# Optimization experiments

Hardware: AMD Instinct MI355X
Metric: run time of the kernel (lower is better)

## Reference

```python
import jax, jax.numpy as jnp
import numpy as np

HEADS = 16
CHUNK = 128  # chunked (mathematically exact) form of the causal cumsum linear attention
EPS = 0.001


def _linear_attention(q, k, v):
    # q, k, v: (B, H, L, d); q, k already SiLU-featurized
    B, H, L, d = q.shape
    Nc = L // CHUNK
    qc = q.reshape(B, H, Nc, CHUNK, d)
    kc = k.reshape(B, H, Nc, CHUNK, d)
    vc = v.reshape(B, H, Nc, CHUNK, d)

    # inter-chunk running state: S = cumsum of k (x) v over previous chunks, z = cumsum of k
    kv_chunk = jnp.einsum('bhncd,bhnce->bhnde', kc, vc)        # (B,H,Nc,d,d)
    S = jnp.cumsum(kv_chunk, axis=2) - kv_chunk                 # exclusive cumsum
    k_sum = kc.sum(axis=3)                                      # (B,H,Nc,d)
    z = jnp.cumsum(k_sum, axis=2) - k_sum                       # exclusive cumsum

    # intra-chunk causal part
    scores = jnp.einsum('bhnid,bhnjd->bhnij', qc, kc)           # (B,H,Nc,C,C)
    mask = jnp.tril(jnp.ones((CHUNK, CHUNK), dtype=bool))
    scores = jnp.where(mask, scores, jnp.zeros((), scores.dtype))
    num = jnp.einsum('bhnij,bhnje->bhnie', scores, vc)
    num = num + jnp.einsum('bhnid,bhnde->bhnie', qc, S)

    k_cum_local = jnp.cumsum(kc, axis=3)                        # within-chunk cumsum of k
    den = jnp.einsum('bhnid,bhnid->bhni', qc, k_cum_local)
    den = den + jnp.einsum('bhnid,bhnd->bhni', qc, z)

    out = num / jnp.maximum(den, EPS)[..., None]
    return out.reshape(B, H, L, d)


def setup_inputs() -> dict:
    key = jax.random.key(0)
    ks = jax.random.split(key, 9)
    D = 1024
    B, L = 4, 2048
    s = 0.02  # init scale
    return {
        'x':  jax.random.normal(ks[0], (B, L, D), dtype=jnp.float32),
        'Wq': jax.random.normal(ks[1], (D, D), dtype=jnp.float32) * s,
        'bq': jnp.zeros((D,), dtype=jnp.float32),
        'Wk': jax.random.normal(ks[2], (D, D), dtype=jnp.float32) * s,
        'bk': jnp.zeros((D,), dtype=jnp.float32),
        'Wv': jax.random.normal(ks[3], (D, D), dtype=jnp.float32) * s,
        'bv': jnp.zeros((D,), dtype=jnp.float32),
        'Wo': jax.random.normal(ks[4], (D, D), dtype=jnp.float32) * s,
        'bo': jnp.zeros((D,), dtype=jnp.float32),
    }


def reference(x, Wq, bq, Wk, bk, Wv, bv, Wo, bo):
    B, L, D = x.shape
    H = HEADS
    d = D // H
    # torch Linear: y = x @ W.T + b
    q = jax.nn.silu(x @ Wq.T + bq).reshape(B, L, H, d).transpose(0, 2, 1, 3)
    k = jax.nn.silu(x @ Wk.T + bk).reshape(B, L, H, d).transpose(0, 2, 1, 3)
    v = (x @ Wv.T + bv).reshape(B, L, H, d).transpose(0, 2, 1, 3)
    out = _linear_attention(q, k, v)                  # (B,H,L,d)
    out = out.transpose(0, 2, 1, 3).reshape(B, L, D)
    return out @ Wo.T + bo
```

## Files before the change

### kernel.cpp

```cpp
#include <hip/hip_runtime.h>
#include <math.h>

#define D_MODEL 1024
#define HEADS   16
#define HDIM    64
#define CHUNK   128
#define B_SZ    4
#define L_SEQ   2048
#define NCHUNK  16
#define NTOK    8192
#define EPS_DEN 1e-3f

typedef _Float16 half8 __attribute__((ext_vector_type(8)));
typedef _Float16 half4 __attribute__((ext_vector_type(4)));
typedef float    f32x4 __attribute__((ext_vector_type(4)));

__device__ __forceinline__ void gld_lds16(const void* g, void* l) {
    __builtin_amdgcn_global_load_lds(
        (const __attribute__((address_space(1))) void*)g,
        (__attribute__((address_space(3))) void*)l, 16, 0, 0);
}

__global__ __launch_bounds__(256) void prep(
    const float* __restrict__ x,  const float* __restrict__ Wq,
    const float* __restrict__ Wk, const float* __restrict__ Wv,
    const float* __restrict__ Wo, const float* __restrict__ bq,
    const float* __restrict__ bk,
    _Float16* __restrict__ x2,  _Float16* __restrict__ w2q,
    _Float16* __restrict__ w2k, _Float16* __restrict__ wv16,
    _Float16* __restrict__ wo16, float* __restrict__ bqk) {
    const int bid = blockIdx.x;
    if (bid < 5120) {
        const float* src; _Float16* dst; int t;
        if (bid < 4096)      { src = x;  dst = x2;  t = bid * 256 + threadIdx.x; }
        else if (bid < 4608) { src = Wq; dst = w2q; t = (bid - 4096) * 256 + threadIdx.x; }
        else                 { src = Wk; dst = w2k; t = (bid - 4608) * 256 + threadIdx.x; }
        int m = t >> 7, kc = (t & 127) << 3;
        const float* s = src + (size_t)m * 1024 + kc;
        f32x4 a = *(const f32x4*)s;
        f32x4 b = *(const f32x4*)(s + 4);
        float xs[8] = {a.x, a.y, a.z, a.w, b.x, b.y, b.z, b.w};
        half8 hi, lo;
        #pragma unroll
        for (int u = 0; u < 8; ++u) {
            _Float16 h = (_Float16)xs[u];
            hi[u] = h;
            lo[u] = (_Float16)(xs[u] - (float)h);
        }
        *(half8*)(dst + (size_t)m * 2048 + kc)        = hi;
        *(half8*)(dst + (size_t)m * 2048 + 1024 + kc) = lo;
    } else if (bid < 6144) {
        const float* src; _Float16* dst; int t;
        if (bid < 5632) { src = Wv; dst = wv16; t = (bid - 5120) * 256 + threadIdx.x; }
        else            { src = Wo; dst = wo16; t = (bid - 5632) * 256 + threadIdx.x; }
        int m = t >> 7, kc = (t & 127) << 3;
        const float* s = src + (size_t)m * 1024 + kc;
        f32x4 a = *(const f32x4*)s;
        f32x4 b = *(const f32x4*)(s + 4);
        float xs[8] = {a.x, a.y, a.z, a.w, b.x, b.y, b.z, b.w};
        half8 hv;
        #pragma unroll
        for (int u = 0; u < 8; ++u) hv[u] = (_Float16)xs[u];
        *(half8*)(dst + (size_t)m * 1024 + kc) = hv;
    } else {
        int i = (bid - 6144) * 256 + threadIdx.x;
        bqk[i] = (i < 1024) ? bq[i] : bk[i - 1024];
    }
}

__global__ __launch_bounds__(256, 4) void gemm_qkv(
    const _Float16* __restrict__ A,
    const _Float16* __restrict__ Bqk,
    const _Float16* __restrict__ Bv,
    const float* __restrict__ bqk, const float* __restrict__ bv,
    _Float16* __restrict__ Qlo, _Float16* __restrict__ Klo,
    _Float16* __restrict__ Q16, _Float16* __restrict__ K16,
    _Float16* __restrict__ V16, float* __restrict__ ksum) {
    __shared__ __align__(16) _Float16 sA[4096];
    __shared__ __align__(16) _Float16 sB[4096];
    __shared__ __align__(16) _Float16 sC16[32 * 136];
    __shared__ float sksum[2][128];

    const int cb   = blockIdx.y;
    const int isqk = (cb < 16);
    const int isk  = (cb >= 8 && cb < 16);
    const int tid  = threadIdx.x;
    const int lane = tid & 63;
    const int w    = tid >> 6;
    const int row0 = blockIdx.x * 128;
    const int col0 = cb * 128;
    const int wm   = (w & 1) * 64;
    const int wn   = (w >> 1) * 64;

    const _Float16* B = isqk ? Bqk : Bv;
    const int ldb     = isqk ? 2048 : 1024;
    const int bcol0   = isqk ? col0 : col0 - 2048;
    const int kits    = isqk ? 96 : 32;

    const int ch0 = w * 64 + lane;
    const int rS0 = ch0 >> 2;
    const int cS0 = (ch0 & 3) ^ ((rS0 >> 1) & 3);
    const int ch1 = ch0 + 256;
    const int rS1 = ch1 >> 2;
    const int cS1 = (ch1 & 3) ^ ((rS1 >> 1) & 3);

    f32x4 acc[4][4];
    #pragma unroll
    for (int i = 0; i < 4; ++i)
        #pragma unroll
        for (int j = 0; j < 4; ++j) { f32x4 z = {0.f, 0.f, 0.f, 0.f}; acc[i][j] = z; }

    const int ml = lane & 15;
    const int kg = lane >> 4;
    int offA[4], offB[4];
    #pragma unroll
    for (int i = 0; i < 4; ++i) {
        int r  = wm + i * 16 + ml;
        offA[i] = r * 32 + (kg ^ ((r >> 1) & 3)) * 8;
        int rn = wn + i * 16 + ml;
        offB[i] = rn * 32 + (kg ^ ((rn >> 1) & 3)) * 8;
    }

    for (int kit = 0; kit < kits; ++kit) {
        const int k0   = kit * 32;
        const int acol = (k0 < 2048) ? k0 : k0 - 2048;
        const int bcol = (k0 < 1024) ? k0 : k0 - 1024;

        gld_lds16(A + (size_t)(row0 + rS0) * 2048 + acol + cS0 * 8, &sA[w * 512]);
        gld_lds16(A + (size_t)(row0 + rS1) * 2048 + acol + cS1 * 8, &sA[2048 + w * 512]);
        gld_lds16(B + (size_t)(bcol0 + rS0) * ldb + bcol + cS0 * 8, &sB[w * 512]);
        gld_lds16(B + (size_t)(bcol0 + rS1) * ldb + bcol + cS1 * 8, &sB[2048 + w * 512]);
        __syncthreads();

        half8 af[4], bf[4];
        #pragma unroll
        for (int i = 0; i < 4; ++i) {
            af[i] = *(const half8*)&sA[offA[i]];
            bf[i] = *(const half8*)&sB[offB[i]];
        }
        #pragma unroll
        for (int i = 0; i < 4; ++i)
            #pragma unroll
            for (int j = 0; j < 4; ++j)
                acc[i][j] = __builtin_amdgcn_mfma_f32_16x16x32_f16(af[i], bf[j], acc[i][j], 0, 0, 0);
        __syncthreads();
    }

    const int colq = isqk ? ((col0 < 1024) ? col0 : col0 - 1024) : (col0 - 2048);
    _Float16* Ylo  = (col0 < 1024) ? Qlo : Klo;
    _Float16* Y16  = isqk ? ((col0 < 1024) ? Q16 : K16) : V16;

    const int rg = lane >> 4;
    #pragma unroll
    for (int j = 0; j < 4; ++j) {
        const float bvb = isqk ? bqk[col0 + wn + j * 16 + ml]
                               : bv[colq + wn + j * 16 + ml];
        const int nn = colq + wn + j * 16 + ml;
        #pragma unroll
        for (int i = 0; i < 4; ++i) {
            #pragma unroll
            for (int t = 0; t < 4; ++t) {
                float vv = acc[i][j][t] + bvb;
                if (isqk) {
                    vv = vv / (1.f + expf(-vv));
                    int mm = row0 + wm + i * 16 + rg * 4 + t;
                    _Float16 hv = (_Float16)vv;
                    Ylo[(size_t)mm * 1024 + nn] = (_Float16)(vv - (float)hv);
                }
                acc[i][j][t] = vv;
            }
        }
    }

    if (isk) {
        #pragma unroll
        for (int j = 0; j < 4; ++j) {
            float ps = 0.f;
            #pragma unroll
            for (int i = 0; i < 4; ++i)
                #pragma unroll
                for (int t = 0; t < 4; ++t) ps += acc[i][j][t];
            ps += __shfl_xor(ps, 16, 64);
            ps += __shfl_xor(ps, 32, 64);
            if (kg == 0) sksum[wm >> 6][wn + j * 16 + ml] = ps;
        }
        __syncthreads();
        if (tid < 128) {
            const int b = row0 >> 11;
            const int n = (row0 >> 7) & 15;
            const int cg = colq + tid;
            const int h = cg >> 6, f = cg & 63;
            ksum[(size_t)(((b * 16 + h) * 16 + n)) * 64 + f] =
                sksum[0][tid] + sksum[1][tid];
        }
        __syncthreads();
    }

    for (int s = 0; s < 4; ++s) {
        if ((wm == 0) == (s < 2)) {
            const int ib = (s & 1) * 2;
            #pragma unroll
            for (int ii = 0; ii < 2; ++ii)
                #pragma unroll
                for (int j = 0; j < 4; ++j)
                    #pragma unroll
                    for (int t = 0; t < 4; ++t) {
                        int lr = ii * 16 + rg * 4 + t;
                        sC16[lr * 136 + wn + j * 16 + ml] = (_Float16)acc[ib + ii][j][t];
                    }
        }
        __syncthreads();
        #pragma unroll
        for (int u = 0; u < 2; ++u) {
            int c = u * 256 + tid;
            int r = c >> 4, cc = (c & 15) * 8;
            half8 hv = *(const half8*)&sC16[r * 136 + cc];
            *(half8*)(Y16 + (size_t)(row0 + 32 * s + r) * 1024 + colq + cc) = hv;
        }
        __syncthreads();
    }
}

__global__ __launch_bounds__(256, 4) void gemm_out(
    const _Float16* __restrict__ A,
    const _Float16* __restrict__ B,
    const float* __restrict__ bias,
    float* __restrict__ Y) {
    __shared__ __align__(16) _Float16 sA[4096];
    __shared__ __align__(16) _Float16 sB[4096];

    const int tid  = threadIdx.x;
    const int lane = tid & 63;
    const int w    = tid >> 6;
    const int row0 = blockIdx.x * 128;
    const int col0 = blockIdx.y * 128;
    const int wm   = (w & 1) * 64;
    const int wn   = (w >> 1) * 64;

    const int ch0 = w * 64 + lane;
    const int rS0 = ch0 >> 2;
    const int cS0 = (ch0 & 3) ^ ((rS0 >> 1) & 3);
    const int ch1 = ch0 + 256;
    const int rS1 = ch1 >> 2;
    const int cS1 = (ch1 & 3) ^ ((rS1 >> 1) & 3);

    f32x4 acc[4][4];
    #pragma unroll
    for (int i = 0; i < 4; ++i)
        #pragma unroll
        for (int j = 0; j < 4; ++j) { f32x4 z = {0.f, 0.f, 0.f, 0.f}; acc[i][j] = z; }

    const int ml = lane & 15;
    const int kg = lane >> 4;
    int offA[4], offB[4];
    #pragma unroll
    for (int i = 0; i < 4; ++i) {
        int r  = wm + i * 16 + ml;
        offA[i] = r * 32 + (kg ^ ((r >> 1) & 3)) * 8;
        int rn = wn + i * 16 + ml;
        offB[i] = rn * 32 + (kg ^ ((rn >> 1) & 3)) * 8;
    }

    for (int kit = 0; kit < 32; ++kit) {
        const int k0 = kit * 32;
        gld_lds16(A + (size_t)(row0 + rS0) * 1024 + k0 + cS0 * 8, &sA[w * 512]);
        gld_lds16(A + (size_t)(row0 + rS1) * 1024 + k0 + cS1 * 8, &sA[2048 + w * 512]);
        gld_lds16(B + (size_t)(col0 + rS0) * 1024 + k0 + cS0 * 8, &sB[w * 512]);
        gld_lds16(B + (size_t)(col0 + rS1) * 1024 + k0 + cS1 * 8, &sB[2048 + w * 512]);
        __syncthreads();

        half8 af[4], bf[4];
        #pragma unroll
        for (int i = 0; i < 4; ++i) {
            af[i] = *(const half8*)&sA[offA[i]];
            bf[i] = *(const half8*)&sB[offB[i]];
        }
        #pragma unroll
        for (int i = 0; i < 4; ++i)
            #pragma unroll
            for (int j = 0; j < 4; ++j)
                acc[i][j] = __builtin_amdgcn_mfma_f32_16x16x32_f16(af[i], bf[j], acc[i][j], 0, 0, 0);
        __syncthreads();
    }

    const int rg = lane >> 4;
    #pragma unroll
    for (int j = 0; j < 4; ++j) {
        const int nn = col0 + wn + j * 16 + ml;
        const float bvb = bias[nn];
        #pragma unroll
        for (int i = 0; i < 4; ++i) {
            #pragma unroll
            for (int t = 0; t < 4; ++t) {
                int mm = row0 + wm + i * 16 + rg * 4 + t;
                Y[(size_t)mm * 1024 + nn] = acc[i][j][t] * 64.f + bvb;
            }
        }
    }
}

__global__ __launch_bounds__(256) void chunk_stats(
    const _Float16* __restrict__ k16g, const _Float16* __restrict__ v16g,
    float* __restrict__ kvT) {
    const int blk = blockIdx.x;
    const int n = blk & 15, bh = blk >> 4, h = bh & 15, b = bh >> 4;
    const size_t base = ((size_t)b * L_SEQ + (size_t)n * CHUNK) * D_MODEL + (size_t)h * HDIM;

    __shared__ __align__(16) _Float16 sv[64 * 136];
    __shared__ __align__(16) _Float16 sk[64 * 136];

    const int tid = threadIdx.x;
    #pragma unroll
    for (int p = 0; p < 4; ++p) {
        int idx = p * 256 + tid;
        int j = idx >> 3, c = idx & 7;
        half8 vv = *(const half8*)(v16g + base + (size_t)j * D_MODEL + c * 8);
        half8 kk = *(const half8*)(k16g + base + (size_t)j * D_MODEL + c * 8);
        #pragma unroll
        for (int u = 0; u < 8; ++u) {
            sv[(c * 8 + u) * 136 + j] = vv[u];
            sk[(c * 8 + u) * 136 + j] = kk[u];
        }
    }
    __syncthreads();

    const int lane = tid & 63;
    const int w    = tid >> 6;
    const int ml   = lane & 15;
    const int kg   = lane >> 4;

    f32x4 acc[4];
    #pragma unroll
    for (int ft = 0; ft < 4; ++ft) { f32x4 z = {0.f,0.f,0.f,0.f}; acc[ft] = z; }
    #pragma unroll
    for (int ft = 0; ft < 4; ++ft)
        #pragma unroll
        for (int kit = 0; kit < 4; ++kit) {
            half8 af = *(const half8*)&sv[(w * 16 + ml) * 136 + kit * 32 + kg * 8];
            half8 bf = *(const half8*)&sk[(ft * 16 + ml) * 136 + kit * 32 + kg * 8];
            acc[ft] = __builtin_amdgcn_mfma_f32_16x16x32_f16(af, bf, acc[ft], 0, 0, 0);
        }
    float* o = kvT + (size_t)blk * 4096;
    #pragma unroll
    for (int ft = 0; ft < 4; ++ft)
        #pragma unroll
        for (int t = 0; t < 4; ++t) {
            int e = w * 16 + kg * 4 + t;
            o[e * 64 + ft * 16 + ml] = acc[ft][t];
        }
}

__global__ __launch_bounds__(256) void scan_chunks(float* __restrict__ kvT,
                                                   float* __restrict__ ksum) {
    const int bh  = blockIdx.x >> 4;
    const int seg = blockIdx.x & 15;
    const int idx = seg * 256 + threadIdx.x;
    float* base = kvT + (size_t)bh * NCHUNK * 4096 + idx;
    float run = 0.f;
    #pragma unroll
    for (int nn = 0; nn < NCHUNK; ++nn) {
        float t = base[(size_t)nn * 4096];
        base[(size_t)nn * 4096] = run;
        run += t;
    }
    if (seg == 0 && threadIdx.x < 64) {
        float* zb = ksum + (size_t)bh * NCHUNK * 64 + threadIdx.x;
        float r2 = 0.f;
        #pragma unroll
        for (int nn = 0; nn < NCHUNK; ++nn) {
            float t = zb[nn * 64];
            zb[nn * 64] = r2;
            r2 += t;
        }
    }
}

__global__ __launch_bounds__(256) void attn_core(
    const _Float16* __restrict__ q16g, const _Float16* __restrict__ k16g,
    const _Float16* __restrict__ v16g, const _Float16* __restrict__ qlog,
    const _Float16* __restrict__ klog, const float* __restrict__ STg,
    const float* __restrict__ zg, _Float16* __restrict__ O16) {
    const int blk = blockIdx.x;
    const int n = blk & 15, bh = blk >> 4, h = bh & 15, b = bh >> 4;
    const size_t base = ((size_t)b * L_SEQ + (size_t)n * CHUNK) * D_MODEL + (size_t)h * HDIM;

    __shared__ __align__(16) _Float16 sq [128 * 72];
    __shared__ __align__(16) _Float16 sk [128 * 72];
    __shared__ __align__(16) _Float16 sv [64 * 136];
    __shared__ __align__(16) _Float16 sS [64 * 72];
    __shared__ __align__(16) _Float16 ssc[64 * 136];
    __shared__ float szz[64];

    const int tid = threadIdx.x;
    #pragma unroll
    for (int p = 0; p < 4; ++p) {
        int idx = p * 256 + tid;
        int j = idx >> 3, c = idx & 7;
        *(half8*)&sq[j * 72 + c * 8] = *(const half8*)(q16g + base + (size_t)j * D_MODEL + c * 8);
        *(half8*)&sk[j * 72 + c * 8] = *(const half8*)(k16g + base + (size_t)j * D_MODEL + c * 8);
        half8 vv = *(const half8*)(v16g + base + (size_t)j * D_MODEL + c * 8);
        #pragma unroll
        for (int u = 0; u < 8; ++u) sv[(c * 8 + u) * 136 + j] = vv[u];
    }
    #pragma unroll
    for (int p = 0; p < 2; ++p) {
        int idx = p * 256 + tid;
        int e = idx >> 3, c = idx & 7;
        f32x4 a = *(const f32x4*)(STg + (size_t)blk * 4096 + e * 64 + c * 8);
        f32x4 b4 = *(const f32x4*)(STg + (size_t)blk * 4096 + e * 64 + c * 8 + 4);
        half8 hv;
        hv[0] = (_Float16)a.x;  hv[1] = (_Float16)a.y;
        hv[2] = (_Float16)a.z;  hv[3] = (_Float16)a.w;
        hv[4] = (_Float16)b4.x; hv[5] = (_Float16)b4.y;
        hv[6] = (_Float16)b4.z; hv[7] = (_Float16)b4.w;
        *(half8*)&sS[e * 72 + c * 8] = hv;
    }
    if (tid < 64) szz[tid] = zg[(size_t)blk * 64 + tid];
    __syncthreads();

    const int lane = tid & 63;
    const int w    = tid >> 6;
    const int ml   = lane & 15;
    const int kg   = lane >> 4;

    for (int h2 = 0; h2 < 2; ++h2) {
        const int r0 = h2 * 64 + w * 16;
        const int rowmax = r0 + 15;

        half8 aflo[2];
        aflo[0] = *(const half8*)(qlog + base + (size_t)(r0 + ml) * D_MODEL + kg * 8);
        aflo[1] = *(const half8*)(qlog + base + (size_t)(r0 + ml) * D_MODEL + 32 + kg * 8);

        f32x4 acc1[8];
        #pragma unroll
        for (int nt = 0; nt < 8; ++nt) { f32x4 z = {0.f,0.f,0.f,0.f}; acc1[nt] = z; }
        #pragma unroll
        for (int nt = 0; nt < 8; ++nt) {
            if (nt * 16 <= rowmax) {
                #pragma unroll
                for (int kit = 0; kit < 2; ++kit) {
                    half8 af = *(const half8*)&sq[(r0 + ml) * 72 + kit * 32 + kg * 8];
                    half8 bf = *(const half8*)&sk[(nt * 16 + ml) * 72 + kit * 32 + kg * 8];
                    acc1[nt] = __builtin_amdgcn_mfma_f32_16x16x32_f16(af, bf, acc1[nt], 0, 0, 0);
                }
            }
        }
        #pragma unroll
        for (int nt = 0; nt < 8; ++nt) {
            if (nt * 16 <= rowmax) {
                const _Float16* kb = klog + base + (size_t)(nt * 16 + ml) * D_MODEL;
                half8 bl0 = *(const half8*)(kb + kg * 8);
                half8 bl1 = *(const half8*)(kb + 32 + kg * 8);
                half8 ah0 = *(const half8*)&sq[(r0 + ml) * 72 + kg * 8];
                half8 ah1 = *(const half8*)&sq[(r0 + ml) * 72 + 32 + kg * 8];
                half8 bh0 = *(const half8*)&sk[(nt * 16 + ml) * 72 + kg * 8];
                half8 bh1 = *(const half8*)&sk[(nt * 16 + ml) * 72 + 32 + kg * 8];
                acc1[nt] = __builtin_amdgcn_mfma_f32_16x16x32_f16(ah0, bl0, acc1[nt], 0, 0, 0);
                acc1[nt] = __builtin_amdgcn_mfma_f32_16x16x32_f16(ah1, bl1, acc1[nt], 0, 0, 0);
                acc1[nt] = __builtin_amdgcn_mfma_f32_16x16x32_f16(aflo[0], bh0, acc1[nt], 0, 0, 0);
                acc1[nt] = __builtin_amdgcn_mfma_f32_16x16x32_f16(aflo[1], bh1, acc1[nt], 0, 0, 0);
            }
        }

        float rs[4];
        #pragma unroll
        for (int t = 0; t < 4; ++t) {
            const int ig = r0 + kg * 4 + t;
            float s = 0.f;
            #pragma unroll
            for (int nt = 0; nt < 8; ++nt) {
                int jg = nt * 16 + ml;
                s += (jg <= ig) ? acc1[nt][t] : 0.f;
            }
            const int f0 = ml * 4;
            half4 ql = *(const half4*)(qlog + base + (size_t)ig * D_MODEL + f0);
            #pragma unroll
            for (int u = 0; u < 4; ++u)
                s += ((float)sq[ig * 72 + f0 + u] + (float)ql[u]) * szz[f0 + u];
            s += __shfl_xor(s, 1, 64);
            s += __shfl_xor(s, 2, 64);
            s += __shfl_xor(s, 4, 64);
            s += __shfl_xor(s, 8, 64);
            rs[t] = s;
        }

        #pragma unroll
        for (int nt = 0; nt < 8; ++nt) {
            #pragma unroll
            for (int t = 0; t < 4; ++t) {
                int lr = w * 16 + kg * 4 + t;
                int ig = h2 * 64 + lr;
                int jg = nt * 16 + ml;
                float val = (jg <= ig) ? acc1[nt][t] : 0.f;
                ssc[lr * 136 + jg] = (_Float16)val;
            }
        }
        __syncthreads();

        f32x4 acc2[4];
        #pragma unroll
        for (int et = 0; et < 4; ++et) { f32x4 z = {0.f,0.f,0.f,0.f}; acc2[et] = z; }
        const int nkit = (h2 == 0) ? 2 : 4;
        #pragma unroll
        for (int et = 0; et < 4; ++et) {
            for (int kit = 0; kit < nkit; ++kit) {
                half8 af = *(const half8*)&ssc[(w * 16 + ml) * 136 + kit * 32 + kg * 8];
                half8 bf = *(const half8*)&sv[(et * 16 + ml) * 136 + kit * 32 + kg * 8];
                acc2[et] = __builtin_amdgcn_mfma_f32_16x16x32_f16(af, bf, acc2[et], 0, 0, 0);
            }
            #pragma unroll
            for (int kit = 0; kit < 2; ++kit) {
                half8 af = *(const half8*)&sq[(r0 + ml) * 72 + kit * 32 + kg * 8];
                half8 bf = *(const half8*)&sS[(et * 16 + ml) * 72 + kit * 32 + kg * 8];
                acc2[et] = __builtin_amdgcn_mfma_f32_16x16x32_f16(af, bf, acc2[et], 0, 0, 0);
            }
        }
        #pragma unroll
        for (int t = 0; t < 4; ++t) {
            int lr = w * 16 + kg * 4 + t;
            int ig = h2 * 64 + lr;
            float rc = 0.015625f / fmaxf(rs[t], EPS_DEN);
            #pragma unroll
            for (int et = 0; et < 4; ++et) {
                int e = et * 16 + ml;
                O16[base + (size_t)ig * D_MODEL + e] = (_Float16)(acc2[et][t] * rc);
            }
        }
        __syncthreads();
    }
}

extern "C" void kernel_launch(void* const* d_in, const int* in_sizes, int n_in,
                              void* d_out, int out_size, void* d_ws, size_t ws_size,
                              hipStream_t stream) {
    const float* x  = (const float*)d_in[0];
    const float* Wq = (const float*)d_in[1];
    const float* bq = (const float*)d_in[2];
    const float* Wk = (const float*)d_in[3];
    const float* bk = (const float*)d_in[4];
    const float* Wv = (const float*)d_in[5];
    const float* bv = (const float*)d_in[6];
    const float* Wo = (const float*)d_in[7];
    const float* bo = (const float*)d_in[8];
    float* out = (float*)d_out;

    char* p = (char*)d_ws;
    _Float16* x2   = (_Float16*)p;  p += (size_t)NTOK * 2048 * 2;
    _Float16* w2q  = (_Float16*)p;  p += (size_t)1024 * 2048 * 2;
    _Float16* w2k  = (_Float16*)p;  p += (size_t)1024 * 2048 * 2;
    _Float16* wv16 = (_Float16*)p;  p += (size_t)1024 * 1024 * 2;
    _Float16* wo16 = (_Float16*)p;  p += (size_t)1024 * 1024 * 2;
    _Float16* qlo  = (_Float16*)p;  p += (size_t)NTOK * 1024 * 2;
    _Float16* klo  = (_Float16*)p;  p += (size_t)NTOK * 1024 * 2;
    _Float16* q16  = (_Float16*)p;  p += (size_t)NTOK * 1024 * 2;
    _Float16* k16  = (_Float16*)p;  p += (size_t)NTOK * 1024 * 2;
    _Float16* v16  = (_Float16*)p;  p += (size_t)NTOK * 1024 * 2;
    float* kvT  = (float*)p;        p += (size_t)1024 * 4096 * 4;
    float* ksb  = (float*)p;        p += (size_t)1024 * 64 * 4;
    float* bqk  = (float*)p;        p += 2048 * 4;
    _Float16* attn16 = x2;

    prep<<<6152, 256, 0, stream>>>(x, Wq, Wk, Wv, Wo, bq, bk,
                                   x2, w2q, w2k, wv16, wo16, bqk);

    gemm_qkv<<<dim3(64, 24), 256, 0, stream>>>(x2, w2q, wv16, bqk, bv,
                                               qlo, klo, q16, k16, v16, ksb);

    chunk_stats<<<1024, 256, 0, stream>>>(k16, v16, kvT);
    scan_chunks<<<1024, 256, 0, stream>>>(kvT, ksb);
    attn_core<<<1024, 256, 0, stream>>>(q16, k16, v16, qlo, klo, kvT, ksb, attn16);

    gemm_out<<<dim3(64, 8), 256, 0, stream>>>(attn16, wo16, bo, out);
}
```

Measured before the change: 346.6 us.

## Restructure QKV GEMM into 256x256 tiles with triple-buffered async LDS pipeline

The QKV projection kernel moves from 128x128 tiles with 256 threads to 256x256 tiles with 512 threads. Each block computes a Q or K tile and then a 128-column V tile, which reuses the A rows and shrinks the grid to 256 blocks. The K loop now uses a three-slot LDS ring filled by global_load_lds, with manual vmcnt waits, split staging between MFMA halves, and setprio around the MFMA bursts, so loads overlap compute. The aim is higher arithmetic intensity and hidden memory latency. The cost is heavier register pressure (128 accumulator floats per thread), fewer blocks than CUs, and fragile hand-written barrier and waitcnt logic.

```diff
diff --git a/kernel.cpp b/kernel.cpp
--- a/kernel.cpp
+++ b/kernel.cpp
@@ -68,7 +68,7 @@
     }
 }
 
-__global__ __launch_bounds__(256, 4) void gemm_qkv(
+__global__ __launch_bounds__(512, 2) void gemm_qkv(
     const _Float16* __restrict__ A,
     const _Float16* __restrict__ Bqk,
     const _Float16* __restrict__ Bv,
@@ -76,148 +76,262 @@
     _Float16* __restrict__ Qlo, _Float16* __restrict__ Klo,
     _Float16* __restrict__ Q16, _Float16* __restrict__ K16,
     _Float16* __restrict__ V16, float* __restrict__ ksum) {
-    __shared__ __align__(16) _Float16 sA[4096];
-    __shared__ __align__(16) _Float16 sB[4096];
-    __shared__ __align__(16) _Float16 sC16[32 * 136];
-    __shared__ float sksum[2][128];
-
-    const int cb   = blockIdx.y;
-    const int isqk = (cb < 16);
-    const int isk  = (cb >= 8 && cb < 16);
+    __shared__ __align__(16) _Float16 sbuf[3 * 16384];
+
     const int tid  = threadIdx.x;
     const int lane = tid & 63;
     const int w    = tid >> 6;
-    const int row0 = blockIdx.x * 128;
-    const int col0 = cb * 128;
-    const int wm   = (w & 1) * 64;
+    const int bx   = blockIdx.x;
+    const int cb   = blockIdx.y;
+    const int row0 = bx * 256;
+    const int col0 = cb * 256;
+    const int isk  = (cb >= 4);
+    const int wm   = (w & 1) * 128;
     const int wn   = (w >> 1) * 64;
-
-    const _Float16* B = isqk ? Bqk : Bv;
-    const int ldb     = isqk ? 2048 : 1024;
-    const int bcol0   = isqk ? col0 : col0 - 2048;
-    const int kits    = isqk ? 96 : 32;
-
-    const int ch0 = w * 64 + lane;
-    const int rS0 = ch0 >> 2;
-    const int cS0 = (ch0 & 3) ^ ((rS0 >> 1) & 3);
-    const int ch1 = ch0 + 256;
-    const int rS1 = ch1 >> 2;
-    const int cS1 = (ch1 & 3) ^ ((rS1 >> 1) & 3);
-
-    f32x4 acc[4][4];
-    #pragma unroll
-    for (int i = 0; i < 4; ++i)
-        #pragma unroll
-        for (int j = 0; j < 4; ++j) { f32x4 z = {0.f, 0.f, 0.f, 0.f}; acc[i][j] = z; }
-
-    const int ml = lane & 15;
-    const int kg = lane >> 4;
-    int offA[4], offB[4];
-    #pragma unroll
-    for (int i = 0; i < 4; ++i) {
-        int r  = wm + i * 16 + ml;
+    const int wnv  = (w >> 1) * 32;
+    const int ml   = lane & 15;
+    const int kg   = lane >> 4;
+
+    const int rS = tid >> 2;
+    const int cS = (tid & 3) ^ ((rS >> 1) & 3);
+    const _Float16* gA0 = A   + (size_t)(row0 + rS) * 2048 + cS * 8;
+    const _Float16* gA1 = gA0 + (size_t)128 * 2048;
+    const _Float16* gB0 = Bqk + (size_t)(col0 + rS) * 2048 + cS * 8;
+    const _Float16* gB1 = gB0 + (size_t)128 * 2048;
+    const _Float16* gBv = Bv  + (size_t)(cb * 128 + rS) * 1024 + cS * 8;
+
+    int offA[8], offB[4], offBv[2];
+    #pragma unroll
+    for (int i = 0; i < 8; ++i) {
+        int r = wm + i * 16 + ml;
         offA[i] = r * 32 + (kg ^ ((r >> 1) & 3)) * 8;
-        int rn = wn + i * 16 + ml;
-        offB[i] = rn * 32 + (kg ^ ((rn >> 1) & 3)) * 8;
-    }
-
-    for (int kit = 0; kit < kits; ++kit) {
-        const int k0   = kit * 32;
+    }
+    #pragma unroll
+    for (int j = 0; j < 4; ++j) {
+        int rn = wn + j * 16 + ml;
+        offB[j] = 8192 + rn * 32 + (kg ^ ((rn >> 1) & 3)) * 8;
+    }
+    #pragma unroll
+    for (int j = 0; j < 2; ++j) {
+        int rn = wnv + j * 16 + ml;
+        offBv[j] = 8192 + rn * 32 + (kg ^ ((rn >> 1) & 3)) * 8;
+    }
+
+    f32x4 acc[8][4];
+    #pragma unroll
+    for (int i = 0; i < 8; ++i)
+        #pragma unroll
+        for (int j = 0; j < 4; ++j) { f32x4 z = {0.f,0.f,0.f,0.f}; acc[i][j] = z; }
+
+    auto stageQK_A = [&](int t, int slot) {
+        const int k0 = t * 32;
         const int acol = (k0 < 2048) ? k0 : k0 - 2048;
+        _Float16* l = sbuf + slot * 16384 + w * 512;
+        gld_lds16(gA0 + acol, l);
+        gld_lds16(gA1 + acol, l + 4096);
+    };
+    auto stageQK_B = [&](int t, int slot) {
+        const int k0 = t * 32;
         const int bcol = (k0 < 1024) ? k0 : k0 - 1024;
-
-        gld_lds16(A + (size_t)(row0 + rS0) * 2048 + acol + cS0 * 8, &sA[w * 512]);
-        gld_lds16(A + (size_t)(row0 + rS1) * 2048 + acol + cS1 * 8, &sA[2048 + w * 512]);
-        gld_lds16(B + (size_t)(bcol0 + rS0) * ldb + bcol + cS0 * 8, &sB[w * 512]);
-        gld_lds16(B + (size_t)(bcol0 + rS1) * ldb + bcol + cS1 * 8, &sB[2048 + w * 512]);
-        __syncthreads();
-
+        _Float16* l = sbuf + slot * 16384 + w * 512;
+        gld_lds16(gB0 + bcol, l + 8192);
+        gld_lds16(gB1 + bcol, l + 12288);
+    };
+
+    stageQK_A(0, 0); stageQK_B(0, 0);
+    stageQK_A(1, 1); stageQK_B(1, 1);
+    int slr = 0, sln = 2;
+    for (int t = 0; t < 96; ++t) {
+        if (t + 1 < 96) asm volatile("s_waitcnt vmcnt(4)\n\ts_barrier" ::: "memory");
+        else            asm volatile("s_waitcnt vmcnt(0)\n\ts_barrier" ::: "memory");
+        const _Float16* lb = sbuf + slr * 16384;
         half8 af[4], bf[4];
         #pragma unroll
-        for (int i = 0; i < 4; ++i) {
-            af[i] = *(const half8*)&sA[offA[i]];
-            bf[i] = *(const half8*)&sB[offB[i]];
-        }
+        for (int i = 0; i < 4; ++i) af[i] = *(const half8*)&lb[offA[i]];
+        #pragma unroll
+        for (int j = 0; j < 4; ++j) bf[j] = *(const half8*)&lb[offB[j]];
+        if (t + 2 < 96) stageQK_A(t + 2, sln);
+        asm volatile("s_barrier" ::: "memory");
+        __builtin_amdgcn_s_setprio(1);
         #pragma unroll
         for (int i = 0; i < 4; ++i)
             #pragma unroll
             for (int j = 0; j < 4; ++j)
                 acc[i][j] = __builtin_amdgcn_mfma_f32_16x16x32_f16(af[i], bf[j], acc[i][j], 0, 0, 0);
-        __syncthreads();
-    }
-
-    const int colq = isqk ? ((col0 < 1024) ? col0 : col0 - 1024) : (col0 - 2048);
-    _Float16* Ylo  = (col0 < 1024) ? Qlo : Klo;
-    _Float16* Y16  = isqk ? ((col0 < 1024) ? Q16 : K16) : V16;
-
-    const int rg = lane >> 4;
+        __builtin_amdgcn_s_setprio(0);
+        asm volatile("s_barrier" ::: "memory");
+        half8 ag[4];
+        #pragma unroll
+        for (int i = 0; i < 4; ++i) ag[i] = *(const half8*)&lb[offA[4 + i]];
+        if (t + 2 < 96) stageQK_B(t + 2, sln);
+        asm volatile("s_barrier" ::: "memory");
+        __builtin_amdgcn_s_setprio(1);
+        #pragma unroll
+        for (int i = 0; i < 4; ++i)
+            #pragma unroll
+            for (int j = 0; j < 4; ++j)
+                acc[4 + i][j] = __builtin_amdgcn_mfma_f32_16x16x32_f16(ag[i], bf[j], acc[4 + i][j], 0, 0, 0);
+        __builtin_amdgcn_s_setprio(0);
+        slr = (slr == 2) ? 0 : slr + 1;
+        sln = (sln == 2) ? 0 : sln + 1;
+    }
+
+    auto stageV_A = [&](int t, int slot) {
+        const int k0 = t * 32;
+        _Float16* l = sbuf + slot * 16384 + w * 512;
+        gld_lds16(gA0 + k0, l);
+        gld_lds16(gA1 + k0, l + 4096);
+    };
+    auto stageV_B = [&](int t, int slot) {
+        gld_lds16(gBv + t * 32, sbuf + slot * 16384 + 8192 + w * 512);
+    };
+    stageV_A(0, 0); stageV_B(0, 0);
+    stageV_A(1, 1); stageV_B(1, 1);
+
+    const int colq = isk ? col0 - 1024 : col0;
+    _Float16* Ylo  = isk ? Klo : Qlo;
+    _Float16* Y16  = isk ? K16 : Q16;
+
     #pragma unroll
     for (int j = 0; j < 4; ++j) {
-        const float bvb = isqk ? bqk[col0 + wn + j * 16 + ml]
-                               : bv[colq + wn + j * 16 + ml];
+        const float bvb = bqk[col0 + wn + j * 16 + ml];
         const int nn = colq + wn + j * 16 + ml;
         #pragma unroll
-        for (int i = 0; i < 4; ++i) {
-            #pragma unroll
-            for (int t = 0; t < 4; ++t) {
-                float vv = acc[i][j][t] + bvb;
-                if (isqk) {
-                    vv = vv / (1.f + expf(-vv));
-                    int mm = row0 + wm + i * 16 + rg * 4 + t;
-                    _Float16 hv = (_Float16)vv;
-                    Ylo[(size_t)mm * 1024 + nn] = (_Float16)(vv - (float)hv);
-                }
-                acc[i][j][t] = vv;
+        for (int i = 0; i < 8; ++i) {
+            #pragma unroll
+            for (int tt = 0; tt < 4; ++tt) {
+                float vv = acc[i][j][tt] + bvb;
+                vv = vv / (1.f + expf(-vv));
+                int mm = row0 + wm + i * 16 + kg * 4 + tt;
+                _Float16 hv = (_Float16)vv;
+                Ylo[(size_t)mm * 1024 + nn] = (_Float16)(vv - (float)hv);
+                acc[i][j][tt] = vv;
             }
         }
     }
 
     if (isk) {
+        const int bb = (row0 + wm) >> 11;
+        const int nc = ((row0 + wm) >> 7) & 15;
         #pragma unroll
         for (int j = 0; j < 4; ++j) {
             float ps = 0.f;
             #pragma unroll
-            for (int i = 0; i < 4; ++i)
+            for (int i = 0; i < 8; ++i)
                 #pragma unroll
-                for (int t = 0; t < 4; ++t) ps += acc[i][j][t];
+                for (int tt = 0; tt < 4; ++tt) ps += acc[i][j][tt];
             ps += __shfl_xor(ps, 16, 64);
             ps += __shfl_xor(ps, 32, 64);
-            if (kg == 0) sksum[wm >> 6][wn + j * 16 + ml] = ps;
-        }
-        __syncthreads();
-        if (tid < 128) {
-            const int b = row0 >> 11;
-            const int n = (row0 >> 7) & 15;
-            const int cg = colq + tid;
-            const int h = cg >> 6, f = cg & 63;
-            ksum[(size_t)(((b * 16 + h) * 16 + n)) * 64 + f] =
-                sksum[0][tid] + sksum[1][tid];
-        }
-        __syncthreads();
-    }
-
-    for (int s = 0; s < 4; ++s) {
-        if ((wm == 0) == (s < 2)) {
-            const int ib = (s & 1) * 2;
-            #pragma unroll
-            for (int ii = 0; ii < 2; ++ii)
+            if (kg == 0) {
+                const int cg = colq + wn + j * 16 + ml;
+                const int h = cg >> 6, f = cg & 63;
+                ksum[(size_t)((bb * 16 + h) * 16 + nc) * 64 + f] = ps;
+            }
+        }
+    }
+
+    {
+        _Float16* sl = sbuf + 32768;
+        asm volatile("s_barrier" ::: "memory");
+        for (int s = 0; s < 8; ++s) {
+            if ((w & 1) == (s >> 2)) {
+                const int i0 = (s & 3) * 2;
                 #pragma unroll
-                for (int j = 0; j < 4; ++j)
+                for (int ii = 0; ii < 2; ++ii)
                     #pragma unroll
-                    for (int t = 0; t < 4; ++t) {
-                        int lr = ii * 16 + rg * 4 + t;
-                        sC16[lr * 136 + wn + j * 16 + ml] = (_Float16)acc[ib + ii][j][t];
-                    }
-        }
-        __syncthreads();
-        #pragma unroll
-        for (int u = 0; u < 2; ++u) {
-            int c = u * 256 + tid;
-            int r = c >> 4, cc = (c & 15) * 8;
-            half8 hv = *(const half8*)&sC16[r * 136 + cc];
-            *(half8*)(Y16 + (size_t)(row0 + 32 * s + r) * 1024 + colq + cc) = hv;
-        }
-        __syncthreads();
+                    for (int j = 0; j < 4; ++j)
+                        #pragma unroll
+                        for (int tt = 0; tt < 4; ++tt) {
+                            int lr = ii * 16 + kg * 4 + tt;
+                            sl[lr * 264 + wn + j * 16 + ml] = (_Float16)acc[i0 + ii][j][tt];
+                        }
+            }
+            __syncthreads();
+            {
+                const int r = tid >> 4, c0 = (tid & 15) * 16;
+                half8 h0 = *(const half8*)&sl[r * 264 + c0];
+                half8 h1 = *(const half8*)&sl[r * 264 + c0 + 8];
+                *(half8*)(Y16 + (size_t)(row0 + s * 32 + r) * 1024 + colq + c0)     = h0;
+                *(half8*)(Y16 + (size_t)(row0 + s * 32 + r) * 1024 + colq + c0 + 8) = h1;
+            }
+            __syncthreads();
+        }
+    }
+
+    f32x4 vacc[8][2];
+    #pragma unroll
+    for (int i = 0; i < 8; ++i)
+        #pragma unroll
+        for (int j = 0; j < 2; ++j) { f32x4 z = {0.f,0.f,0.f,0.f}; vacc[i][j] = z; }
+
+    slr = 0; sln = 2;
+    for (int t = 0; t < 32; ++t) {
+        if (t + 1 < 32) asm volatile("s_waitcnt vmcnt(3)\n\ts_barrier" ::: "memory");
+        else            asm volatile("s_waitcnt vmcnt(0)\n\ts_barrier" ::: "memory");
+        const _Float16* lb = sbuf + slr * 16384;
+        half8 af[4], bf[2];
+        #pragma unroll
+        for (int i = 0; i < 4; ++i) af[i] = *(const half8*)&lb[offA[i]];
+        #pragma unroll
+        for (int j = 0; j < 2; ++j) bf[j] = *(const half8*)&lb[offBv[j]];
+        if (t + 2 < 32) stageV_A(t + 2, sln);
+        asm volatile("s_barrier" ::: "memory");
+        __builtin_amdgcn_s_setprio(1);
+        #pragma unroll
+        for (int i = 0; i < 4; ++i)
+            #pragma unroll
+            for (int j = 0; j < 2; ++j)
+                vacc[i][j] = __builtin_amdgcn_mfma_f32_16x16x32_f16(af[i], bf[j], vacc[i][j], 0, 0, 0);
+        __builtin_amdgcn_s_setprio(0);
+        asm volatile("s_barrier" ::: "memory");
+        half8 ag[4];
+        #pragma unroll
+        for (int i = 0; i < 4; ++i) ag[i] = *(const half8*)&lb[offA[4 + i]];
+        if (t + 2 < 32) stageV_B(t + 2, sln);
+        asm volatile("s_barrier" ::: "memory");
+        __builtin_amdgcn_s_setprio(1);
+        #pragma unroll
+        for (int i = 0; i < 4; ++i)
+            #pragma unroll
+            for (int j = 0; j < 2; ++j)
+                vacc[4 + i][j] = __builtin_amdgcn_mfma_f32_16x16x32_f16(ag[i], bf[j], vacc[4 + i][j], 0, 0, 0);
+        __builtin_amdgcn_s_setprio(0);
+        slr = (slr == 2) ? 0 : slr + 1;
+        sln = (sln == 2) ? 0 : sln + 1;
+    }
+
+    #pragma unroll
+    for (int j = 0; j < 2; ++j) {
+        const float bvb = bv[cb * 128 + wnv + j * 16 + ml];
+        #pragma unroll
+        for (int i = 0; i < 8; ++i)
+            #pragma unroll
+            for (int tt = 0; tt < 4; ++tt) vacc[i][j][tt] += bvb;
+    }
+    {
+        _Float16* sl = sbuf + 32768;
+        asm volatile("s_barrier" ::: "memory");
+        for (int s = 0; s < 8; ++s) {
+            if ((w & 1) == (s >> 2)) {
+                const int i0 = (s & 3) * 2;
+                #pragma unroll
+                for (int ii = 0; ii < 2; ++ii)
+                    #pragma unroll
+                    for (int j = 0; j < 2; ++j)
+                        #pragma unroll
+                        for (int tt = 0; tt < 4; ++tt) {
+                            int lr = ii * 16 + kg * 4 + tt;
+                            sl[lr * 136 + wnv + j * 16 + ml] = (_Float16)vacc[i0 + ii][j][tt];
+                        }
+            }
+            __syncthreads();
+            {
+                const int r = tid >> 4, c0 = (tid & 15) * 8;
+                half8 h0 = *(const half8*)&sl[r * 136 + c0];
+                *(half8*)(V16 + (size_t)(row0 + s * 32 + r) * 1024 + cb * 128 + c0) = h0;
+            }
+            __syncthreads();
+        }
     }
 }
 
@@ -563,8 +677,8 @@
     prep<<<6152, 256, 0, stream>>>(x, Wq, Wk, Wv, Wo, bq, bk,
                                    x2, w2q, w2k, wv16, wo16, bqk);
 
-    gemm_qkv<<<dim3(64, 24), 256, 0, stream>>>(x2, w2q, wv16, bqk, bv,
-                                               qlo, klo, q16, k16, v16, ksb);
+    gemm_qkv<<<dim3(32, 8), 512, 0, stream>>>(x2, w2q, wv16, bqk, bv,
+                                              qlo, klo, q16, k16, v16, ksb);
 
     chunk_stats<<<1024, 256, 0, stream>>>(k16, v16, kvT);
     scan_chunks<<<1024, 256, 0, stream>>>(kvT, ksb);
```

Result: slower. 355.8 us (+2.7%).

## Double-buffer LDS tiles in QKV and output GEMMs to overlap loads with MFMA

Applied to the files above, without the earlier changes.

Both GEMM kernels now use two LDS buffers and issue the direct global-to-LDS loads for the next k-tile before running the MFMAs on the current tile. Each iteration then ends with a single vmcnt wait plus barrier instead of two __syncthreads. This is meant to hide global load latency behind matrix math. s_setprio is also raised around the MFMA block. LDS use per block doubles to 32KB, which may limit occupancy under the 4-blocks-per-CU launch bound. There is also a possible hazard from reading the current buffer while the epilogue's sC16 aliases the same LDS.

```diff
diff --git a/kernel.cpp b/kernel.cpp
--- a/kernel.cpp
+++ b/kernel.cpp
@@ -76,10 +76,9 @@
     _Float16* __restrict__ Qlo, _Float16* __restrict__ Klo,
     _Float16* __restrict__ Q16, _Float16* __restrict__ K16,
     _Float16* __restrict__ V16, float* __restrict__ ksum) {
-    __shared__ __align__(16) _Float16 sA[4096];
-    __shared__ __align__(16) _Float16 sB[4096];
-    __shared__ __align__(16) _Float16 sC16[32 * 136];
+    __shared__ __align__(16) _Float16 sbuf[2 * 8192];
     __shared__ float sksum[2][128];
+    _Float16* sC16 = sbuf;
 
     const int cb   = blockIdx.y;
     const int isqk = (cb < 16);
@@ -104,6 +103,22 @@
     const int rS1 = ch1 >> 2;
     const int cS1 = (ch1 & 3) ^ ((rS1 >> 1) & 3);
 
+    const _Float16* gA0 = A + (size_t)(row0  + rS0) * 2048 + cS0 * 8;
+    const _Float16* gA1 = A + (size_t)(row0  + rS1) * 2048 + cS1 * 8;
+    const _Float16* gB0 = B + (size_t)(bcol0 + rS0) * ldb  + cS0 * 8;
+    const _Float16* gB1 = B + (size_t)(bcol0 + rS1) * ldb  + cS1 * 8;
+
+    auto stage = [&](int kt, int bsel) {
+        const int k0   = kt * 32;
+        const int acol = (k0 < 2048) ? k0 : k0 - 2048;
+        const int bcol = (k0 < 1024) ? k0 : k0 - 1024;
+        _Float16* l = sbuf + bsel * 8192;
+        gld_lds16(gA0 + acol, l + w * 512);
+        gld_lds16(gA1 + acol, l + 2048 + w * 512);
+        gld_lds16(gB0 + bcol, l + 4096 + w * 512);
+        gld_lds16(gB1 + bcol, l + 6144 + w * 512);
+    };
+
     f32x4 acc[4][4];
     #pragma unroll
     for (int i = 0; i < 4; ++i)
@@ -118,32 +133,30 @@
         int r  = wm + i * 16 + ml;
         offA[i] = r * 32 + (kg ^ ((r >> 1) & 3)) * 8;
         int rn = wn + i * 16 + ml;
-        offB[i] = rn * 32 + (kg ^ ((rn >> 1) & 3)) * 8;
-    }
-
-    for (int kit = 0; kit < kits; ++kit) {
-        const int k0   = kit * 32;
-        const int acol = (k0 < 2048) ? k0 : k0 - 2048;
-        const int bcol = (k0 < 1024) ? k0 : k0 - 1024;
-
-        gld_lds16(A + (size_t)(row0 + rS0) * 2048 + acol + cS0 * 8, &sA[w * 512]);
-        gld_lds16(A + (size_t)(row0 + rS1) * 2048 + acol + cS1 * 8, &sA[2048 + w * 512]);
-        gld_lds16(B + (size_t)(bcol0 + rS0) * ldb + bcol + cS0 * 8, &sB[w * 512]);
-        gld_lds16(B + (size_t)(bcol0 + rS1) * ldb + bcol + cS1 * 8, &sB[2048 + w * 512]);
-        __syncthreads();
-
+        offB[i] = 4096 + rn * 32 + (kg ^ ((rn >> 1) & 3)) * 8;
+    }
+
+    stage(0, 0);
+    asm volatile("s_waitcnt vmcnt(0)\n\ts_barrier" ::: "memory");
+    int cur = 0;
+    for (int t = 0; t < kits; ++t) {
+        if (t + 1 < kits) stage(t + 1, cur ^ 1);
+        const _Float16* lb = sbuf + cur * 8192;
         half8 af[4], bf[4];
         #pragma unroll
         for (int i = 0; i < 4; ++i) {
-            af[i] = *(const half8*)&sA[offA[i]];
-            bf[i] = *(const half8*)&sB[offB[i]];
-        }
+            af[i] = *(const half8*)&lb[offA[i]];
+            bf[i] = *(const half8*)&lb[offB[i]];
+        }
+        __builtin_amdgcn_s_setprio(1);
         #pragma unroll
         for (int i = 0; i < 4; ++i)
             #pragma unroll
             for (int j = 0; j < 4; ++j)
                 acc[i][j] = __builtin_amdgcn_mfma_f32_16x16x32_f16(af[i], bf[j], acc[i][j], 0, 0, 0);
-        __syncthreads();
+        __builtin_amdgcn_s_setprio(0);
+        asm volatile("s_waitcnt vmcnt(0)\n\ts_barrier" ::: "memory");
+        cur ^= 1;
     }
 
     const int colq = isqk ? ((col0 < 1024) ? col0 : col0 - 1024) : (col0 - 2048);
@@ -226,8 +239,7 @@
     const _Float16* __restrict__ B,
     const float* __restrict__ bias,
     float* __restrict__ Y) {
-    __shared__ __align__(16) _Float16 sA[4096];
-    __shared__ __align__(16) _Float16 sB[4096];
+    __shared__ __align__(16) _Float16 sbuf[2 * 8192];
 
     const int tid  = threadIdx.x;
     const int lane = tid & 63;
@@ -244,6 +256,20 @@
     const int rS1 = ch1 >> 2;
     const int cS1 = (ch1 & 3) ^ ((rS1 >> 1) & 3);
 
+    const _Float16* gA0 = A + (size_t)(row0 + rS0) * 1024 + cS0 * 8;
+    const _Float16* gA1 = A + (size_t)(row0 + rS1) * 1024 + cS1 * 8;
+    const _Float16* gB0 = B + (size_t)(col0 + rS0) * 1024 + cS0 * 8;
+    const _Float16* gB1 = B + (size_t)(col0 + rS1) * 1024 + cS1 * 8;
+
+    auto stage = [&](int kt, int bsel) {
+        const int k0 = kt * 32;
+        _Float16* l = sbuf + bsel * 8192;
+        gld_lds16(gA0 + k0, l + w * 512);
+        gld_lds16(gA1 + k0, l + 2048 + w * 512);
+        gld_lds16(gB0 + k0, l + 4096 + w * 512);
+        gld_lds16(gB1 + k0, l + 6144 + w * 512);
+    };
+
     f32x4 acc[4][4];
     #pragma unroll
     for (int i = 0; i < 4; ++i)
@@ -258,29 +284,30 @@
         int r  = wm + i * 16 + ml;
         offA[i] = r * 32 + (kg ^ ((r >> 1) & 3)) * 8;
         int rn = wn + i * 16 + ml;
-        offB[i] = rn * 32 + (kg ^ ((rn >> 1) & 3)) * 8;
-    }
-
+        offB[i] = 4096 + rn * 32 + (kg ^ ((rn >> 1) & 3)) * 8;
+    }
+
+    stage(0, 0);
+    asm volatile("s_waitcnt vmcnt(0)\n\ts_barrier" ::: "memory");
+    int cur = 0;
     for (int kit = 0; kit < 32; ++kit) {
-        const int k0 = kit * 32;
-        gld_lds16(A + (size_t)(row0 + rS0) * 1024 + k0 + cS0 * 8, &sA[w * 512]);
-        gld_lds16(A + (size_t)(row0 + rS1) * 1024 + k0 + cS1 * 8, &sA[2048 + w * 512]);
-        gld_lds16(B + (size_t)(col0 + rS0) * 1024 + k0 + cS0 * 8, &sB[w * 512]);
-        gld_lds16(B + (size_t)(col0 + rS1) * 1024 + k0 + cS1 * 8, &sB[2048 + w * 512]);
-        __syncthreads();
-
+        if (kit + 1 < 32) stage(kit + 1, cur ^ 1);
+        const _Float16* lb = sbuf + cur * 8192;
         half8 af[4], bf[4];
         #pragma unroll
         for (int i = 0; i < 4; ++i) {
-            af[i] = *(const half8*)&sA[offA[i]];
-            bf[i] = *(const half8*)&sB[offB[i]];
-        }
+            af[i] = *(const half8*)&lb[offA[i]];
+            bf[i] = *(const half8*)&lb[offB[i]];
+        }
+        __builtin_amdgcn_s_setprio(1);
         #pragma unroll
         for (int i = 0; i < 4; ++i)
             #pragma unroll
             for (int j = 0; j < 4; ++j)
                 acc[i][j] = __builtin_amdgcn_mfma_f32_16x16x32_f16(af[i], bf[j], acc[i][j], 0, 0, 0);
-        __syncthreads();
+        __builtin_amdgcn_s_setprio(0);
+        asm volatile("s_waitcnt vmcnt(0)\n\ts_barrier" ::: "memory");
+        cur ^= 1;
     }
 
     const int rg = lane >> 4;
```

Measured after the change: 338.6 us. -2.3%, faster.
